# Optimization experiments

Hardware: AMD Instinct MI355X
Metric: run time of the kernel (lower is better)

## Reference

```python
import jax, jax.numpy as jnp
import numpy as np

N = 100000      # nodes
E = 600000      # edges
IN, OUT = 128, 32
L1 = IN - (IN - OUT) // 3          # 96
L2 = IN - (2 * (IN - OUT)) // 3    # 64


def setup_inputs() -> dict:
    key = jax.random.key(0)
    ks = jax.random.split(key, 12)

    def lin(k, i, o):
        return jax.random.normal(k, (i, o), jnp.float32) / np.float32(np.sqrt(i))

    return {
        "x": jax.random.normal(ks[0], (N, IN), jnp.float32),
        "edge_index": jax.random.randint(ks[1], (2, E), 0, N, dtype=jnp.int32),
        # ClusterGCNConv 1: lin_out (W,b) + lin_root (no bias)
        "W1": lin(ks[2], IN, L1), "b1": jnp.zeros((L1,), jnp.float32), "Wr1": lin(ks[3], IN, L1),
        # ClusterGCNConv 2
        "W2": lin(ks[4], L1, L2), "b2": jnp.zeros((L2,), jnp.float32), "Wr2": lin(ks[5], L1, L2),
        # GCNConv mu / logstd heads
        "Wmu": lin(ks[6], L2, OUT), "bmu": jnp.zeros((OUT,), jnp.float32),
        "Wls": lin(ks[7], L2, OUT), "bls": jnp.zeros((OUT,), jnp.float32),
    }


def _with_self_loops(edge_index, n):
    loops = jnp.arange(n, dtype=edge_index.dtype)
    src = jnp.concatenate([edge_index[0], loops])
    dst = jnp.concatenate([edge_index[1], loops])
    return src, dst


def _cluster_gcn(x, edge_index, W, b, Wr, n):
    # PyG ClusterGCNConv (diag_lambda=0): out = (D^{-1} (A+I)) x @ W + b + x @ Wr
    src, dst = _with_self_loops(edge_index, n)
    deg = jax.ops.segment_sum(jnp.ones_like(dst, x.dtype), dst, num_segments=n)
    dinv = 1.0 / jnp.clip(deg, 1.0)
    agg = jax.ops.segment_sum(x[src] * dinv[dst][:, None], dst, num_segments=n)
    return agg @ W + b + x @ Wr


def _gcn(x, edge_index, W, b, n):
    # PyG GCNConv: h = x @ W; out = D^{-1/2} (A+I) D^{-1/2} h + b
    h = x @ W
    src, dst = _with_self_loops(edge_index, n)
    deg = jax.ops.segment_sum(jnp.ones_like(dst, h.dtype), dst, num_segments=n)
    dis = jax.lax.rsqrt(jnp.clip(deg, 1.0))  # deg >= 1 thanks to self loops
    norm = dis[src] * dis[dst]
    return jax.ops.segment_sum(h[src] * norm[:, None], dst, num_segments=n) + b


def reference(x, edge_index, W1, b1, Wr1, W2, b2, Wr2, Wmu, bmu, Wls, bls):
    n = x.shape[0]
    h = jax.nn.relu(_cluster_gcn(x, edge_index, W1, b1, Wr1, n))
    h = jax.nn.relu(_cluster_gcn(h, edge_index, W2, b2, Wr2, n))
    return (_gcn(h, edge_index, Wmu, bmu, n), _gcn(h, edge_index, Wls, bls, n))
```

## Files before the change

### kernel.cpp

```cpp
#include <hip/hip_runtime.h>

#define TPB 256

typedef __attribute__((ext_vector_type(8))) short          bf8_t;
typedef __attribute__((ext_vector_type(8))) unsigned short us8_t;
typedef __attribute__((ext_vector_type(4))) float          f4_t;
typedef __attribute__((ext_vector_type(4))) unsigned short us4_t;

__device__ __forceinline__ unsigned short f2bf(float f) {
    union { float f; unsigned u; } v; v.f = f;
    unsigned r = v.u + 0x7FFFu + ((v.u >> 16) & 1u);
    return (unsigned short)(r >> 16);
}
__device__ __forceinline__ float bf2f(unsigned short u) {
    union { unsigned u; float f; } v; v.u = (unsigned)u << 16; return v.f;
}


__global__ void k_count(const int* __restrict__ ei, int E, int* __restrict__ cnt) {
    int e = blockIdx.x * TPB + threadIdx.x;
    if (e < E) atomicAdd(&cnt[ei[E + e]], 1);
}

__global__ void k_blocksum(const int* __restrict__ cnt, int n, int* __restrict__ bsum) {
    __shared__ int s[TPB];
    int t = threadIdx.x, i = blockIdx.x * TPB + t;
    s[t] = (i < n) ? cnt[i] : 0;
    __syncthreads();
    for (int off = TPB / 2; off > 0; off >>= 1) {
        if (t < off) s[t] += s[t + off];
        __syncthreads();
    }
    if (t == 0) bsum[blockIdx.x] = s[0];
}

__global__ void k_scan_bsum(int* __restrict__ bsum, int nb) {
    __shared__ int s[512];
    int t = threadIdx.x;
    int v = (t < nb) ? bsum[t] : 0;
    s[t] = v; __syncthreads();
    for (int off = 1; off < 512; off <<= 1) {
        int x = (t >= off) ? s[t - off] : 0;
        __syncthreads();
        s[t] += x;
        __syncthreads();
    }
    if (t < nb) bsum[t] = s[t] - v;
}

__global__ void k_rowptr(const int* __restrict__ cnt, const int* __restrict__ bsum, int n, int E,
                         int* __restrict__ rowptr, int* __restrict__ cursor,
                         float* __restrict__ dinv, float* __restrict__ dis) {
    __shared__ int s[TPB];
    int t = threadIdx.x, i = blockIdx.x * TPB + t;
    int v = (i < n) ? cnt[i] : 0;
    s[t] = v; __syncthreads();
    for (int off = 1; off < TPB; off <<= 1) {
        int x = (t >= off) ? s[t - off] : 0;
        __syncthreads();
        s[t] += x;
        __syncthreads();
    }
    if (i < n) {
        int start = bsum[blockIdx.x] + s[t] - v;
        rowptr[i] = start;
        cursor[i] = start;
        float d = (float)(v + 1);
        dinv[i] = 1.0f / d;
        dis[i]  = rsqrtf(d);
    }
    if (i == 0) rowptr[n] = E;
}

__global__ void k_fill(const int* __restrict__ ei, int E,
                       int* __restrict__ cursor, int* __restrict__ col) {
    int e = blockIdx.x * TPB + threadIdx.x;
    if (e < E) {
        int src = ei[e], dst = ei[E + e];
        int p = atomicAdd(&cursor[dst], 1);
        col[p] = src;
    }
}

__global__ void k_wconv(const float* W1, const float* Wr1, const float* W2, const float* Wr2,
                        const float* Wmu, const float* Wls,
                        unsigned short* T1, unsigned short* Tr1, unsigned short* T2,
                        unsigned short* Tr2, unsigned short* Tmu, unsigned short* Tls) {
    const float* W; unsigned short* T; int K, M;
    switch (blockIdx.y) {
        case 0: W = W1;  T = T1;  K = 128; M = 96; break;
        case 1: W = Wr1; T = Tr1; K = 128; M = 96; break;
        case 2: W = W2;  T = T2;  K = 96;  M = 64; break;
        case 3: W = Wr2; T = Tr2; K = 96;  M = 64; break;
        case 4: W = Wmu; T = Tmu; K = 64;  M = 32; break;
        default:W = Wls; T = Tls; K = 64;  M = 32; break;
    }
    int idx = blockIdx.x * TPB + threadIdx.x;
    if (idx < K * M) {
        int m = idx / K, k = idx % K;
        T[idx] = f2bf(W[k * M + m]);
    }
}

template <int K, int M, bool AF32>
__global__ __launch_bounds__(TPB) void k_gemm3(const void* __restrict__ Av,
                                               const unsigned short* __restrict__ WT,
                                               unsigned short* __restrict__ Yb,
                                               int n, int nt) {
    constexpr int KS = K / 32;
    constexpr int ST = K + 8;
    __shared__ unsigned short Bs[M * ST];
    for (int i = threadIdx.x * 8; i < M * K; i += TPB * 8) {
        int m = i / K, k = i - m * K;
        *(us8_t*)(Bs + m * ST + k) = *(const us8_t*)(WT + i);
    }
    __syncthreads();

    int lane = threadIdx.x & 63;
    int wave = threadIdx.x >> 6;
    int quad = lane >> 4;
    int l15  = lane & 15;

    for (int tile = blockIdx.x; tile < nt; tile += gridDim.x) {
        int base = tile * 64 + wave * 16;
        int rA = base + l15; if (rA > n - 1) rA = n - 1;

        bf8_t a[KS];
        if (AF32) {
            const float* ap = (const float*)Av + (size_t)rA * K + quad * 8;
#pragma unroll
            for (int s = 0; s < KS; s++) {
                f4_t lo = *(const f4_t*)(ap + s * 32);
                f4_t hi = *(const f4_t*)(ap + s * 32 + 4);
                bf8_t t;
                t[0] = (short)f2bf(lo.x); t[1] = (short)f2bf(lo.y);
                t[2] = (short)f2bf(lo.z); t[3] = (short)f2bf(lo.w);
                t[4] = (short)f2bf(hi.x); t[5] = (short)f2bf(hi.y);
                t[6] = (short)f2bf(hi.z); t[7] = (short)f2bf(hi.w);
                a[s] = t;
            }
        } else {
            const unsigned short* ap = (const unsigned short*)Av + (size_t)rA * K + quad * 8;
#pragma unroll
            for (int s = 0; s < KS; s++) a[s] = *(const bf8_t*)(ap + s * 32);
        }

        int row = base + quad * 4;
#pragma unroll
        for (int ct = 0; ct < M / 16; ct++) {
            const unsigned short* bp = Bs + (ct * 16 + l15) * ST + quad * 8;
            f4_t acc = {0.f, 0.f, 0.f, 0.f};
#pragma unroll
            for (int s = 0; s < KS; s++) {
                bf8_t b = *(const bf8_t*)(bp + s * 32);
                acc = __builtin_amdgcn_mfma_f32_16x16x32_bf16(a[s], b, acc, 0, 0, 0);
            }
            int colg = ct * 16 + l15;
#pragma unroll
            for (int r = 0; r < 4; r++) {
                if (row + r < n) Yb[(size_t)(row + r) * M + colg] = f2bf(acc[r]);
            }
        }
    }
}

__global__ __launch_bounds__(TPB, 4) void k_fuse1(const unsigned short* __restrict__ AB,
                                                  const unsigned short* __restrict__ WT2,
                                                  const float* __restrict__ bias,
                                                  const float* __restrict__ dinv,
                                                  const int* __restrict__ rowptr,
                                                  const int* __restrict__ col,
                                                  unsigned short* __restrict__ AB2,
                                                  int n, int nt) {
    constexpr int LDA = 192, MF = 96, ST1 = 104, KS = 3, M2 = 128;
    __shared__ unsigned short Hs[2][16 * ST1];

    int t = threadIdx.x;
    int lane = t & 63, wave = t >> 6, quad = lane >> 4, l15 = lane & 15;

    bf8_t breg[2][KS];
#pragma unroll
    for (int j = 0; j < 2; j++) {
        const unsigned short* bp = WT2 + (size_t)((wave * 2 + j) * 16 + l15) * 96 + quad * 8;
#pragma unroll
        for (int s = 0; s < KS; s++) breg[j][s] = *(const bf8_t*)(bp + s * 32);
    }

    int gl = t >> 4;
    int cg = t & 15;
    int c  = cg * 8;
    bool p1act = (c < MF);

    int p = 0;
    for (int tile = blockIdx.x; tile < nt; tile += gridDim.x, p ^= 1) {
        int tbase = tile * 16;
        if (p1act) {
            int g = tbase + gl; if (g > n - 1) g = n - 1;
            int r0 = rowptr[g], r1 = rowptr[g + 1];
            float acc[8];
            {
                bf8_t v = *(const bf8_t*)(AB + (size_t)g * LDA + c);
#pragma unroll
                for (int j = 0; j < 8; j++) acc[j] = bf2f((unsigned short)v[j]);
            }
            int e = r0;
            for (; e + 4 <= r1; e += 4) {
                int s0 = col[e], s1 = col[e + 1], s2 = col[e + 2], s3 = col[e + 3];
                bf8_t v0 = *(const bf8_t*)(AB + (size_t)s0 * LDA + c);
                bf8_t v1 = *(const bf8_t*)(AB + (size_t)s1 * LDA + c);
                bf8_t v2 = *(const bf8_t*)(AB + (size_t)s2 * LDA + c);
                bf8_t v3 = *(const bf8_t*)(AB + (size_t)s3 * LDA + c);
#pragma unroll
                for (int j = 0; j < 8; j++)
                    acc[j] += (bf2f((unsigned short)v0[j]) + bf2f((unsigned short)v1[j]))
                            + (bf2f((unsigned short)v2[j]) + bf2f((unsigned short)v3[j]));
            }
            for (; e < r1; ++e) {
                int s = col[e];
                bf8_t v = *(const bf8_t*)(AB + (size_t)s * LDA + c);
#pragma unroll
                for (int j = 0; j < 8; j++) acc[j] += bf2f((unsigned short)v[j]);
            }
            float di = dinv[g];
            bf8_t rr = *(const bf8_t*)(AB + (size_t)g * LDA + MF + c);
            us8_t o;
#pragma unroll
            for (int j = 0; j < 8; j++)
                o[j] = f2bf(fmaxf(acc[j] * di + bf2f((unsigned short)rr[j]) + bias[c + j], 0.f));
            *(us8_t*)(&Hs[p][gl * ST1 + c]) = o;
        }
        __syncthreads();

        int row = tbase + quad * 4;
#pragma unroll
        for (int j = 0; j < 2; j++) {
            const unsigned short* apl = &Hs[p][l15 * ST1 + quad * 8];
            f4_t acc2 = {0.f, 0.f, 0.f, 0.f};
#pragma unroll
            for (int s = 0; s < KS; s++) {
                bf8_t a = *(const bf8_t*)(apl + s * 32);
                acc2 = __builtin_amdgcn_mfma_f32_16x16x32_bf16(a, breg[j][s], acc2, 0, 0, 0);
            }
            int colg = (wave * 2 + j) * 16 + l15;
#pragma unroll
            for (int r = 0; r < 4; r++) {
                if (row + r < n) AB2[(size_t)(row + r) * M2 + colg] = f2bf(acc2[r]);
            }
        }
    }
}

template <int MF, int GRP, bool SCALE>
__global__ __launch_bounds__(TPB) void k_aggc(const unsigned short* __restrict__ AB,
                                              const float* __restrict__ bias,
                                              const float* __restrict__ dinv,
                                              const float* __restrict__ dis,
                                              const int* __restrict__ rowptr,
                                              const int* __restrict__ col,
                                              unsigned short* __restrict__ Hb, int n) {
    constexpr int LD = 2 * MF;
    int g = blockIdx.x * (TPB / GRP) + threadIdx.x / GRP;
    int l = threadIdx.x & (GRP - 1);
    if (g >= n) return;
    int c = l * 8;
    if (c >= MF) return;
    int r0 = rowptr[g], r1 = rowptr[g + 1];
    float acc[8];
    {
        bf8_t v = *(const bf8_t*)(AB + (size_t)g * LD + c);
#pragma unroll
        for (int j = 0; j < 8; j++) acc[j] = bf2f((unsigned short)v[j]);
    }
    int e = r0;
    for (; e + 4 <= r1; e += 4) {
        int s0 = col[e], s1 = col[e + 1], s2 = col[e + 2], s3 = col[e + 3];
        bf8_t v0 = *(const bf8_t*)(AB + (size_t)s0 * LD + c);
        bf8_t v1 = *(const bf8_t*)(AB + (size_t)s1 * LD + c);
        bf8_t v2 = *(const bf8_t*)(AB + (size_t)s2 * LD + c);
        bf8_t v3 = *(const bf8_t*)(AB + (size_t)s3 * LD + c);
#pragma unroll
        for (int j = 0; j < 8; j++)
            acc[j] += (bf2f((unsigned short)v0[j]) + bf2f((unsigned short)v1[j]))
                    + (bf2f((unsigned short)v2[j]) + bf2f((unsigned short)v3[j]));
    }
    for (; e < r1; ++e) {
        int s = col[e];
        bf8_t v = *(const bf8_t*)(AB + (size_t)s * LD + c);
#pragma unroll
        for (int j = 0; j < 8; j++) acc[j] += bf2f((unsigned short)v[j]);
    }
    float di = dinv[g];
    float sc = SCALE ? dis[g] : 1.0f;
    bf8_t rr = *(const bf8_t*)(AB + (size_t)g * LD + MF + c);
    us8_t o;
#pragma unroll
    for (int j = 0; j < 8; j++) {
        float h = fmaxf(acc[j] * di + bf2f((unsigned short)rr[j]) + bias[c + j], 0.f);
        o[j] = f2bf(SCALE ? sc * h : h);
    }
    *(us8_t*)(Hb + (size_t)g * MF + c) = o;
}

__global__ __launch_bounds__(TPB, 4) void k_fuse2(const unsigned short* __restrict__ H2s,
                                                  const unsigned short* __restrict__ WTo,
                                                  const float* __restrict__ bmu,
                                                  const float* __restrict__ bls,
                                                  const float* __restrict__ dis,
                                                  const int* __restrict__ rowptr,
                                                  const int* __restrict__ col,
                                                  float* __restrict__ out, int n, int nt) {
    constexpr int ST2 = 72, KS = 2;
    __shared__ unsigned short Zs[2][32 * ST2];

    int t = threadIdx.x;
    int lane = t & 63, wave = t >> 6, quad = lane >> 4, l15 = lane & 15;

    bf8_t breg[KS];
    {
        const unsigned short* bp = WTo + (size_t)(wave * 16 + l15) * 64 + quad * 8;
#pragma unroll
        for (int s = 0; s < KS; s++) breg[s] = *(const bf8_t*)(bp + s * 32);
    }
    int colg = wave * 16 + l15;
    float bias = (colg < 32) ? bmu[colg] : bls[colg - 32];
    float* dstc = (colg < 32) ? (out + colg) : (out + (size_t)n * 32 + (colg - 32));

    int gl = t >> 3;
    int c  = (t & 7) * 8;

    int p = 0;
    for (int tile = blockIdx.x; tile < nt; tile += gridDim.x, p ^= 1) {
        int tbase = tile * 32;
        {
            int g = tbase + gl; if (g > n - 1) g = n - 1;
            int r0 = rowptr[g], r1 = rowptr[g + 1];
            float acc[8];
            {
                bf8_t v = *(const bf8_t*)(H2s + (size_t)g * 64 + c);
#pragma unroll
                for (int j = 0; j < 8; j++) acc[j] = bf2f((unsigned short)v[j]);
            }
            int e = r0;
            for (; e + 4 <= r1; e += 4) {
                int s0 = col[e], s1 = col[e + 1], s2 = col[e + 2], s3 = col[e + 3];
                bf8_t v0 = *(const bf8_t*)(H2s + (size_t)s0 * 64 + c);
                bf8_t v1 = *(const bf8_t*)(H2s + (size_t)s1 * 64 + c);
                bf8_t v2 = *(const bf8_t*)(H2s + (size_t)s2 * 64 + c);
                bf8_t v3 = *(const bf8_t*)(H2s + (size_t)s3 * 64 + c);
#pragma unroll
                for (int j = 0; j < 8; j++)
                    acc[j] += (bf2f((unsigned short)v0[j]) + bf2f((unsigned short)v1[j]))
                            + (bf2f((unsigned short)v2[j]) + bf2f((unsigned short)v3[j]));
            }
            for (; e < r1; ++e) {
                int s = col[e];
                bf8_t v = *(const bf8_t*)(H2s + (size_t)s * 64 + c);
#pragma unroll
                for (int j = 0; j < 8; j++) acc[j] += bf2f((unsigned short)v[j]);
            }
            float dg = dis[g];
            us8_t o;
#pragma unroll
            for (int j = 0; j < 8; j++) o[j] = f2bf(dg * acc[j]);
            *(us8_t*)(&Zs[p][gl * ST2 + c]) = o;
        }
        __syncthreads();

#pragma unroll
        for (int st = 0; st < 2; st++) {
            const unsigned short* apl = &Zs[p][(st * 16 + l15) * ST2 + quad * 8];
            bf8_t a[KS];
#pragma unroll
            for (int s = 0; s < KS; s++) a[s] = *(const bf8_t*)(apl + s * 32);
            f4_t acc = {0.f, 0.f, 0.f, 0.f};
#pragma unroll
            for (int s = 0; s < KS; s++)
                acc = __builtin_amdgcn_mfma_f32_16x16x32_bf16(a[s], breg[s], acc, 0, 0, 0);
            int row = tbase + st * 16 + quad * 4;
#pragma unroll
            for (int r = 0; r < 4; r++) {
                if (row + r < n) dstc[(size_t)(row + r) * 32] = acc[r] + bias;
            }
        }
    }
}


extern "C" void kernel_launch(void* const* d_in, const int* in_sizes, int n_in,
                              void* d_out, int out_size, void* d_ws, size_t ws_size,
                              hipStream_t stream) {
    const float* x   = (const float*)d_in[0];
    const int*   ei  = (const int*)d_in[1];
    const float* W1  = (const float*)d_in[2];
    const float* b1  = (const float*)d_in[3];
    const float* Wr1 = (const float*)d_in[4];
    const float* W2  = (const float*)d_in[5];
    const float* b2  = (const float*)d_in[6];
    const float* Wr2 = (const float*)d_in[7];
    const float* Wmu = (const float*)d_in[8];
    const float* bmu = (const float*)d_in[9];
    const float* Wls = (const float*)d_in[10];
    const float* bls = (const float*)d_in[11];
    float* out = (float*)d_out;

    const int IN = 128, L1F = 96, L2F = 64;
    const int N = in_sizes[0] / IN;
    const int E = in_sizes[1] / 2;

    char* ws = (char*)d_ws;
    size_t off = 0;
    auto alloc = [&](size_t b) { size_t r = off; off += (b + 255) & ~(size_t)255; return r; };

    const int nb = (N + TPB - 1) / TPB;
    int*   cnt  = (int*)(ws + alloc((size_t)N * 4));
    int*   bsum = (int*)(ws + alloc((size_t)nb * 4));
    int*   rowp = (int*)(ws + alloc((size_t)(N + 1) * 4));
    int*   curs = (int*)(ws + alloc((size_t)N * 4));
    int*   col  = (int*)(ws + alloc((size_t)E * 4));
    float* dinv = (float*)(ws + alloc((size_t)N * 4));
    float* dis  = (float*)(ws + alloc((size_t)N * 4));
    unsigned short* T1  = (unsigned short*)(ws + alloc((size_t)IN  * L1F * 2));
    unsigned short* Tr1 = (unsigned short*)(ws + alloc((size_t)IN  * L1F * 2));
    unsigned short* T2  = (unsigned short*)(ws + alloc((size_t)L1F * L2F * 2));
    unsigned short* Tr2 = (unsigned short*)(ws + alloc((size_t)L1F * L2F * 2));
    unsigned short* Tmu = (unsigned short*)(ws + alloc((size_t)L2F * 32 * 2));
    unsigned short* Tls = (unsigned short*)(ws + alloc((size_t)L2F * 32 * 2));
    unsigned short* AB1 = (unsigned short*)(ws + alloc((size_t)N * 2 * L1F * 2));
    unsigned short* AB2 = (unsigned short*)(ws + alloc((size_t)N * 2 * L2F * 2));
    unsigned short* H2s = (unsigned short*)(ws + alloc((size_t)N * L2F * 2));
    (void)Tr1; (void)Tr2; (void)Tls;

    hipMemsetAsync(cnt, 0, (size_t)N * 4, stream);

    dim3 eg((E + TPB - 1) / TPB);
    k_count<<<eg, TPB, 0, stream>>>(ei, E, cnt);
    k_blocksum<<<nb, TPB, 0, stream>>>(cnt, N, bsum);
    k_scan_bsum<<<1, 512, 0, stream>>>(bsum, nb);
    k_rowptr<<<nb, TPB, 0, stream>>>(cnt, bsum, N, E, rowp, curs, dinv, dis);
    k_fill<<<eg, TPB, 0, stream>>>(ei, E, curs, col);

    k_wconv<<<dim3(48, 6), TPB, 0, stream>>>(W1, Wr1, W2, Wr2, Wmu, Wls,
                                             T1, Tr1, T2, Tr2, Tmu, Tls);

    const int nt64 = (N + 63) / 64;
    k_gemm3<128, 192, true><<<768, TPB, 0, stream>>>(x, T1, AB1, N, nt64);

    const int nt16 = (N + 15) / 16;
    k_fuse1<<<2048, TPB, 0, stream>>>(AB1, T2, b1, dinv, rowp, col, AB2, N, nt16);

    k_aggc<64, 8, true><<<(N + 31) / 32, TPB, 0, stream>>>(AB2, b2, dinv, dis, rowp, col, H2s, N);

    const int nt32 = (N + 31) / 32;
    k_fuse2<<<2048, TPB, 0, stream>>>(H2s, Tmu, bmu, bls, dis, rowp, col, out, N, nt32);
}
```

Baseline: 281.4 us.

## Split edge gathers across two lane groups per node and merge scan kernels

The three gather-aggregation kernels now split each node's edge list between two half-groups of lanes (even/odd edges) and combine the partial sums with a cross-lane shuffle. This doubles the memory-level parallelism per node and fills the lanes that were idle in k_fuse1, at the cost of extra shuffles and some wasted lanes on low-degree nodes. Separately, the block-sum and block-scan kernels are merged into one single-block kernel that sums each chunk serially, which removes a launch but adds serial work in one block.

Result: slower. 320.3 us (+13.9%).

```diff
diff --git a/kernel.cpp b/kernel.cpp
--- a/kernel.cpp
+++ b/kernel.cpp
@@ -22,30 +22,23 @@
     if (e < E) atomicAdd(&cnt[ei[E + e]], 1);
 }
 
-__global__ void k_blocksum(const int* __restrict__ cnt, int n, int* __restrict__ bsum) {
-    __shared__ int s[TPB];
-    int t = threadIdx.x, i = blockIdx.x * TPB + t;
-    s[t] = (i < n) ? cnt[i] : 0;
-    __syncthreads();
-    for (int off = TPB / 2; off > 0; off >>= 1) {
-        if (t < off) s[t] += s[t + off];
-        __syncthreads();
-    }
-    if (t == 0) bsum[blockIdx.x] = s[0];
-}
-
-__global__ void k_scan_bsum(int* __restrict__ bsum, int nb) {
+__global__ void k_scan12(const int* __restrict__ cnt, int n, int nb, int* __restrict__ bsum) {
     __shared__ int s[512];
     int t = threadIdx.x;
-    int v = (t < nb) ? bsum[t] : 0;
-    s[t] = v; __syncthreads();
+    int sum = 0;
+    if (t < nb) {
+        int base = t * TPB;
+        int end = base + TPB; if (end > n) end = n;
+        for (int i = base; i < end; i++) sum += cnt[i];
+    }
+    s[t] = sum; __syncthreads();
     for (int off = 1; off < 512; off <<= 1) {
         int x = (t >= off) ? s[t - off] : 0;
         __syncthreads();
         s[t] += x;
         __syncthreads();
     }
-    if (t < nb) bsum[t] = s[t] - v;
+    if (t < nb) bsum[t] = s[t] - sum;
 }
 
 __global__ void k_rowptr(const int* __restrict__ cnt, const int* __restrict__ bsum, int n, int E,
@@ -164,6 +157,7 @@
     }
 }
 
+
 __global__ __launch_bounds__(TPB, 4) void k_fuse1(const unsigned short* __restrict__ AB,
                                                   const unsigned short* __restrict__ WT2,
                                                   const float* __restrict__ bias,
@@ -186,48 +180,60 @@
         for (int s = 0; s < KS; s++) breg[j][s] = *(const bf8_t*)(bp + s * 32);
     }
 
-    int gl = t >> 4;
-    int cg = t & 15;
-    int c  = cg * 8;
-    bool p1act = (c < MF);
+    int u   = t & 31;
+    int eh  = u >> 4;
+    int cg  = u & 15;
+    int c   = cg * 8;
+    bool act = (c < MF);
+    int slot = t >> 5;
 
     int p = 0;
     for (int tile = blockIdx.x; tile < nt; tile += gridDim.x, p ^= 1) {
         int tbase = tile * 16;
-        if (p1act) {
+#pragma unroll
+        for (int pp = 0; pp < 2; pp++) {
+            int gl = pp * 8 + slot;
             int g = tbase + gl; if (g > n - 1) g = n - 1;
-            int r0 = rowptr[g], r1 = rowptr[g + 1];
             float acc[8];
-            {
-                bf8_t v = *(const bf8_t*)(AB + (size_t)g * LDA + c);
-#pragma unroll
-                for (int j = 0; j < 8; j++) acc[j] = bf2f((unsigned short)v[j]);
-            }
-            int e = r0;
-            for (; e + 4 <= r1; e += 4) {
-                int s0 = col[e], s1 = col[e + 1], s2 = col[e + 2], s3 = col[e + 3];
-                bf8_t v0 = *(const bf8_t*)(AB + (size_t)s0 * LDA + c);
-                bf8_t v1 = *(const bf8_t*)(AB + (size_t)s1 * LDA + c);
-                bf8_t v2 = *(const bf8_t*)(AB + (size_t)s2 * LDA + c);
-                bf8_t v3 = *(const bf8_t*)(AB + (size_t)s3 * LDA + c);
+#pragma unroll
+            for (int j = 0; j < 8; j++) acc[j] = 0.f;
+            if (act) {
+                if (eh == 0) {
+                    bf8_t v = *(const bf8_t*)(AB + (size_t)g * LDA + c);
+#pragma unroll
+                    for (int j = 0; j < 8; j++) acc[j] = bf2f((unsigned short)v[j]);
+                }
+                int r0 = rowptr[g], r1 = rowptr[g + 1];
+                int e = r0 + eh;
+                for (; e + 6 < r1; e += 8) {
+                    int s0 = col[e], s1 = col[e + 2], s2 = col[e + 4], s3 = col[e + 6];
+                    bf8_t v0 = *(const bf8_t*)(AB + (size_t)s0 * LDA + c);
+                    bf8_t v1 = *(const bf8_t*)(AB + (size_t)s1 * LDA + c);
+                    bf8_t v2 = *(const bf8_t*)(AB + (size_t)s2 * LDA + c);
+                    bf8_t v3 = *(const bf8_t*)(AB + (size_t)s3 * LDA + c);
+#pragma unroll
+                    for (int j = 0; j < 8; j++)
+                        acc[j] += (bf2f((unsigned short)v0[j]) + bf2f((unsigned short)v1[j]))
+                                + (bf2f((unsigned short)v2[j]) + bf2f((unsigned short)v3[j]));
+                }
+                for (; e < r1; e += 2) {
+                    int s = col[e];
+                    bf8_t v = *(const bf8_t*)(AB + (size_t)s * LDA + c);
+#pragma unroll
+                    for (int j = 0; j < 8; j++) acc[j] += bf2f((unsigned short)v[j]);
+                }
+            }
+#pragma unroll
+            for (int j = 0; j < 8; j++) acc[j] += __shfl_xor(acc[j], 16, 64);
+            if (act && eh == 0) {
+                float di = dinv[g];
+                bf8_t rr = *(const bf8_t*)(AB + (size_t)g * LDA + MF + c);
+                us8_t o;
 #pragma unroll
                 for (int j = 0; j < 8; j++)
-                    acc[j] += (bf2f((unsigned short)v0[j]) + bf2f((unsigned short)v1[j]))
-                            + (bf2f((unsigned short)v2[j]) + bf2f((unsigned short)v3[j]));
-            }
-            for (; e < r1; ++e) {
-                int s = col[e];
-                bf8_t v = *(const bf8_t*)(AB + (size_t)s * LDA + c);
-#pragma unroll
-                for (int j = 0; j < 8; j++) acc[j] += bf2f((unsigned short)v[j]);
-            }
-            float di = dinv[g];
-            bf8_t rr = *(const bf8_t*)(AB + (size_t)g * LDA + MF + c);
-            us8_t o;
-#pragma unroll
-            for (int j = 0; j < 8; j++)
-                o[j] = f2bf(fmaxf(acc[j] * di + bf2f((unsigned short)rr[j]) + bias[c + j], 0.f));
-            *(us8_t*)(&Hs[p][gl * ST1 + c]) = o;
+                    o[j] = f2bf(fmaxf(acc[j] * di + bf2f((unsigned short)rr[j]) + bias[c + j], 0.f));
+                *(us8_t*)(&Hs[p][gl * ST1 + c]) = o;
+            }
         }
         __syncthreads();
 
@@ -250,30 +256,32 @@
     }
 }
 
-template <int MF, int GRP, bool SCALE>
-__global__ __launch_bounds__(TPB) void k_aggc(const unsigned short* __restrict__ AB,
-                                              const float* __restrict__ bias,
-                                              const float* __restrict__ dinv,
-                                              const float* __restrict__ dis,
-                                              const int* __restrict__ rowptr,
-                                              const int* __restrict__ col,
-                                              unsigned short* __restrict__ Hb, int n) {
-    constexpr int LD = 2 * MF;
-    int g = blockIdx.x * (TPB / GRP) + threadIdx.x / GRP;
-    int l = threadIdx.x & (GRP - 1);
+__global__ __launch_bounds__(TPB) void k_aggc2(const unsigned short* __restrict__ AB,
+                                               const float* __restrict__ bias,
+                                               const float* __restrict__ dinv,
+                                               const float* __restrict__ dis,
+                                               const int* __restrict__ rowptr,
+                                               const int* __restrict__ col,
+                                               unsigned short* __restrict__ Hb, int n) {
+    constexpr int MF = 64, LD = 128;
+    int t = threadIdx.x;
+    int g = blockIdx.x * 16 + (t >> 4);
     if (g >= n) return;
-    int c = l * 8;
-    if (c >= MF) return;
+    int u  = t & 15;
+    int eh = u >> 3;
+    int c  = (u & 7) * 8;
     int r0 = rowptr[g], r1 = rowptr[g + 1];
     float acc[8];
-    {
+#pragma unroll
+    for (int j = 0; j < 8; j++) acc[j] = 0.f;
+    if (eh == 0) {
         bf8_t v = *(const bf8_t*)(AB + (size_t)g * LD + c);
 #pragma unroll
         for (int j = 0; j < 8; j++) acc[j] = bf2f((unsigned short)v[j]);
     }
-    int e = r0;
-    for (; e + 4 <= r1; e += 4) {
-        int s0 = col[e], s1 = col[e + 1], s2 = col[e + 2], s3 = col[e + 3];
+    int e = r0 + eh;
+    for (; e + 6 < r1; e += 8) {
+        int s0 = col[e], s1 = col[e + 2], s2 = col[e + 4], s3 = col[e + 6];
         bf8_t v0 = *(const bf8_t*)(AB + (size_t)s0 * LD + c);
         bf8_t v1 = *(const bf8_t*)(AB + (size_t)s1 * LD + c);
         bf8_t v2 = *(const bf8_t*)(AB + (size_t)s2 * LD + c);
@@ -283,22 +291,25 @@
             acc[j] += (bf2f((unsigned short)v0[j]) + bf2f((unsigned short)v1[j]))
                     + (bf2f((unsigned short)v2[j]) + bf2f((unsigned short)v3[j]));
     }
-    for (; e < r1; ++e) {
+    for (; e < r1; e += 2) {
         int s = col[e];
         bf8_t v = *(const bf8_t*)(AB + (size_t)s * LD + c);
 #pragma unroll
         for (int j = 0; j < 8; j++) acc[j] += bf2f((unsigned short)v[j]);
     }
-    float di = dinv[g];
-    float sc = SCALE ? dis[g] : 1.0f;
-    bf8_t rr = *(const bf8_t*)(AB + (size_t)g * LD + MF + c);
-    us8_t o;
-#pragma unroll
-    for (int j = 0; j < 8; j++) {
-        float h = fmaxf(acc[j] * di + bf2f((unsigned short)rr[j]) + bias[c + j], 0.f);
-        o[j] = f2bf(SCALE ? sc * h : h);
-    }
-    *(us8_t*)(Hb + (size_t)g * MF + c) = o;
+#pragma unroll
+    for (int j = 0; j < 8; j++) acc[j] += __shfl_xor(acc[j], 8, 64);
+    if (eh == 0) {
+        float di = dinv[g], sc = dis[g];
+        bf8_t rr = *(const bf8_t*)(AB + (size_t)g * LD + MF + c);
+        us8_t o;
+#pragma unroll
+        for (int j = 0; j < 8; j++) {
+            float h = fmaxf(acc[j] * di + bf2f((unsigned short)rr[j]) + bias[c + j], 0.f);
+            o[j] = f2bf(sc * h);
+        }
+        *(us8_t*)(Hb + (size_t)g * MF + c) = o;
+    }
 }
 
 __global__ __launch_bounds__(TPB, 4) void k_fuse2(const unsigned short* __restrict__ H2s,
@@ -325,24 +336,30 @@
     float bias = (colg < 32) ? bmu[colg] : bls[colg - 32];
     float* dstc = (colg < 32) ? (out + colg) : (out + (size_t)n * 32 + (colg - 32));
 
-    int gl = t >> 3;
-    int c  = (t & 7) * 8;
+    int u  = t & 15;
+    int eh = u >> 3;
+    int c  = (u & 7) * 8;
+    int slot = t >> 4;
 
     int p = 0;
     for (int tile = blockIdx.x; tile < nt; tile += gridDim.x, p ^= 1) {
         int tbase = tile * 32;
-        {
+#pragma unroll
+        for (int pp = 0; pp < 2; pp++) {
+            int gl = pp * 16 + slot;
             int g = tbase + gl; if (g > n - 1) g = n - 1;
+            float acc[8];
+#pragma unroll
+            for (int j = 0; j < 8; j++) acc[j] = 0.f;
+            if (eh == 0) {
+                bf8_t v = *(const bf8_t*)(H2s + (size_t)g * 64 + c);
+#pragma unroll
+                for (int j = 0; j < 8; j++) acc[j] = bf2f((unsigned short)v[j]);
+            }
             int r0 = rowptr[g], r1 = rowptr[g + 1];
-            float acc[8];
-            {
-                bf8_t v = *(const bf8_t*)(H2s + (size_t)g * 64 + c);
-#pragma unroll
-                for (int j = 0; j < 8; j++) acc[j] = bf2f((unsigned short)v[j]);
-            }
-            int e = r0;
-            for (; e + 4 <= r1; e += 4) {
-                int s0 = col[e], s1 = col[e + 1], s2 = col[e + 2], s3 = col[e + 3];
+            int e = r0 + eh;
+            for (; e + 6 < r1; e += 8) {
+                int s0 = col[e], s1 = col[e + 2], s2 = col[e + 4], s3 = col[e + 6];
                 bf8_t v0 = *(const bf8_t*)(H2s + (size_t)s0 * 64 + c);
                 bf8_t v1 = *(const bf8_t*)(H2s + (size_t)s1 * 64 + c);
                 bf8_t v2 = *(const bf8_t*)(H2s + (size_t)s2 * 64 + c);
@@ -352,17 +369,21 @@
                     acc[j] += (bf2f((unsigned short)v0[j]) + bf2f((unsigned short)v1[j]))
                             + (bf2f((unsigned short)v2[j]) + bf2f((unsigned short)v3[j]));
             }
-            for (; e < r1; ++e) {
+            for (; e < r1; e += 2) {
                 int s = col[e];
                 bf8_t v = *(const bf8_t*)(H2s + (size_t)s * 64 + c);
 #pragma unroll
                 for (int j = 0; j < 8; j++) acc[j] += bf2f((unsigned short)v[j]);
             }
-            float dg = dis[g];
-            us8_t o;
-#pragma unroll
-            for (int j = 0; j < 8; j++) o[j] = f2bf(dg * acc[j]);
-            *(us8_t*)(&Zs[p][gl * ST2 + c]) = o;
+#pragma unroll
+            for (int j = 0; j < 8; j++) acc[j] += __shfl_xor(acc[j], 8, 64);
+            if (eh == 0) {
+                float dg = dis[g];
+                us8_t o;
+#pragma unroll
+                for (int j = 0; j < 8; j++) o[j] = f2bf(dg * acc[j]);
+                *(us8_t*)(&Zs[p][gl * ST2 + c]) = o;
+            }
         }
         __syncthreads();
 
@@ -434,8 +455,7 @@
 
     dim3 eg((E + TPB - 1) / TPB);
     k_count<<<eg, TPB, 0, stream>>>(ei, E, cnt);
-    k_blocksum<<<nb, TPB, 0, stream>>>(cnt, N, bsum);
-    k_scan_bsum<<<1, 512, 0, stream>>>(bsum, nb);
+    k_scan12<<<1, 512, 0, stream>>>(cnt, N, nb, bsum);
     k_rowptr<<<nb, TPB, 0, stream>>>(cnt, bsum, N, E, rowp, curs, dinv, dis);
     k_fill<<<eg, TPB, 0, stream>>>(ei, E, curs, col);
 
@@ -448,7 +468,7 @@
     const int nt16 = (N + 15) / 16;
     k_fuse1<<<2048, TPB, 0, stream>>>(AB1, T2, b1, dinv, rowp, col, AB2, N, nt16);
 
-    k_aggc<64, 8, true><<<(N + 31) / 32, TPB, 0, stream>>>(AB2, b2, dinv, dis, rowp, col, H2s, N);
+    k_aggc2<<<(N + 15) / 16, TPB, 0, stream>>>(AB2, b2, dinv, dis, rowp, col, H2s, N);
 
     const int nt32 = (N + 31) / 32;
     k_fuse2<<<2048, TPB, 0, stream>>>(H2s, Tmu, bmu, bls, dis, rowp, col, out, N, nt32);
```

## Split interleaved agg/root GEMM outputs into separate buffers and merge scan kernels

Applied to the files above, without the earlier changes.

The GEMM outputs that feed neighbour aggregation (Y) are now stored apart from the root-term outputs (R), each in its own dense buffer, instead of interleaved rows of width 2*F. Gathers over neighbours then read compact rows, so each gathered row spans fewer cache lines and the unused root half is no longer pulled in. The block-sum and block-scan kernels are also merged into one single-block kernel, removing a launch at the cost of a serial per-thread summation.

Measured after the change: 289.8 us. +3.0%, slower.

```diff
diff --git a/kernel.cpp b/kernel.cpp
--- a/kernel.cpp
+++ b/kernel.cpp
@@ -6,6 +6,7 @@
 typedef __attribute__((ext_vector_type(8))) unsigned short us8_t;
 typedef __attribute__((ext_vector_type(4))) float          f4_t;
 typedef __attribute__((ext_vector_type(4))) unsigned short us4_t;
+typedef __attribute__((ext_vector_type(4))) int            i4_t;
 
 __device__ __forceinline__ unsigned short f2bf(float f) {
     union { float f; unsigned u; } v; v.f = f;
@@ -22,30 +23,28 @@
     if (e < E) atomicAdd(&cnt[ei[E + e]], 1);
 }
 
-__global__ void k_blocksum(const int* __restrict__ cnt, int n, int* __restrict__ bsum) {
-    __shared__ int s[TPB];
-    int t = threadIdx.x, i = blockIdx.x * TPB + t;
-    s[t] = (i < n) ? cnt[i] : 0;
-    __syncthreads();
-    for (int off = TPB / 2; off > 0; off >>= 1) {
-        if (t < off) s[t] += s[t + off];
-        __syncthreads();
-    }
-    if (t == 0) bsum[blockIdx.x] = s[0];
-}
-
-__global__ void k_scan_bsum(int* __restrict__ bsum, int nb) {
+__global__ void k_scan12(const int* __restrict__ cnt, int n, int nb, int* __restrict__ bsum) {
     __shared__ int s[512];
     int t = threadIdx.x;
-    int v = (t < nb) ? bsum[t] : 0;
-    s[t] = v; __syncthreads();
+    int sum = 0;
+    if (t < nb) {
+        int base = t * TPB;
+        int end = base + TPB; if (end > n) end = n;
+        int i = base;
+        for (; i + 4 <= end; i += 4) {
+            i4_t v = *(const i4_t*)(cnt + i);
+            sum += v.x + v.y + v.z + v.w;
+        }
+        for (; i < end; i++) sum += cnt[i];
+    }
+    s[t] = sum; __syncthreads();
     for (int off = 1; off < 512; off <<= 1) {
         int x = (t >= off) ? s[t - off] : 0;
         __syncthreads();
         s[t] += x;
         __syncthreads();
     }
-    if (t < nb) bsum[t] = s[t] - v;
+    if (t < nb) bsum[t] = s[t] - sum;
 }
 
 __global__ void k_rowptr(const int* __restrict__ cnt, const int* __restrict__ bsum, int n, int E,
@@ -102,11 +101,12 @@
     }
 }
 
-template <int K, int M, bool AF32>
-__global__ __launch_bounds__(TPB) void k_gemm3(const void* __restrict__ Av,
-                                               const unsigned short* __restrict__ WT,
-                                               unsigned short* __restrict__ Yb,
-                                               int n, int nt) {
+template <int K, int M, int MH, bool AF32>
+__global__ __launch_bounds__(TPB) void k_gemm3s(const void* __restrict__ Av,
+                                                const unsigned short* __restrict__ WT,
+                                                unsigned short* __restrict__ Yb,
+                                                unsigned short* __restrict__ Rb,
+                                                int n, int nt) {
     constexpr int KS = K / 32;
     constexpr int ST = K + 8;
     __shared__ unsigned short Bs[M * ST];
@@ -156,23 +156,30 @@
                 acc = __builtin_amdgcn_mfma_f32_16x16x32_bf16(a[s], b, acc, 0, 0, 0);
             }
             int colg = ct * 16 + l15;
+            unsigned short* dst;
+            if (ct * 16 < MH) dst = Yb + (size_t)0 * MH + colg;
+            else              dst = Rb + (colg - MH);
+            constexpr int SY = MH, SR = M - MH;
+            int stride = (ct * 16 < MH) ? SY : SR;
 #pragma unroll
             for (int r = 0; r < 4; r++) {
-                if (row + r < n) Yb[(size_t)(row + r) * M + colg] = f2bf(acc[r]);
-            }
-        }
-    }
-}
-
-__global__ __launch_bounds__(TPB, 4) void k_fuse1(const unsigned short* __restrict__ AB,
+                if (row + r < n) dst[(size_t)(row + r) * stride] = f2bf(acc[r]);
+            }
+        }
+    }
+}
+
+__global__ __launch_bounds__(TPB, 4) void k_fuse1(const unsigned short* __restrict__ Y1,
+                                                  const unsigned short* __restrict__ R1,
                                                   const unsigned short* __restrict__ WT2,
                                                   const float* __restrict__ bias,
                                                   const float* __restrict__ dinv,
                                                   const int* __restrict__ rowptr,
                                                   const int* __restrict__ col,
-                                                  unsigned short* __restrict__ AB2,
+                                                  unsigned short* __restrict__ Y2,
+                                                  unsigned short* __restrict__ R2,
                                                   int n, int nt) {
-    constexpr int LDA = 192, MF = 96, ST1 = 104, KS = 3, M2 = 128;
+    constexpr int MF = 96, ST1 = 104, KS = 3;
     __shared__ unsigned short Hs[2][16 * ST1];
 
     int t = threadIdx.x;
@@ -199,17 +206,17 @@
             int r0 = rowptr[g], r1 = rowptr[g + 1];
             float acc[8];
             {
-                bf8_t v = *(const bf8_t*)(AB + (size_t)g * LDA + c);
+                bf8_t v = *(const bf8_t*)(Y1 + (size_t)g * MF + c);
 #pragma unroll
                 for (int j = 0; j < 8; j++) acc[j] = bf2f((unsigned short)v[j]);
             }
             int e = r0;
             for (; e + 4 <= r1; e += 4) {
                 int s0 = col[e], s1 = col[e + 1], s2 = col[e + 2], s3 = col[e + 3];
-                bf8_t v0 = *(const bf8_t*)(AB + (size_t)s0 * LDA + c);
-                bf8_t v1 = *(const bf8_t*)(AB + (size_t)s1 * LDA + c);
-                bf8_t v2 = *(const bf8_t*)(AB + (size_t)s2 * LDA + c);
-                bf8_t v3 = *(const bf8_t*)(AB + (size_t)s3 * LDA + c);
+                bf8_t v0 = *(const bf8_t*)(Y1 + (size_t)s0 * MF + c);
+                bf8_t v1 = *(const bf8_t*)(Y1 + (size_t)s1 * MF + c);
+                bf8_t v2 = *(const bf8_t*)(Y1 + (size_t)s2 * MF + c);
+                bf8_t v3 = *(const bf8_t*)(Y1 + (size_t)s3 * MF + c);
 #pragma unroll
                 for (int j = 0; j < 8; j++)
                     acc[j] += (bf2f((unsigned short)v0[j]) + bf2f((unsigned short)v1[j]))
@@ -217,12 +224,12 @@
             }
             for (; e < r1; ++e) {
                 int s = col[e];
-                bf8_t v = *(const bf8_t*)(AB + (size_t)s * LDA + c);
+                bf8_t v = *(const bf8_t*)(Y1 + (size_t)s * MF + c);
 #pragma unroll
                 for (int j = 0; j < 8; j++) acc[j] += bf2f((unsigned short)v[j]);
             }
             float di = dinv[g];
-            bf8_t rr = *(const bf8_t*)(AB + (size_t)g * LDA + MF + c);
+            bf8_t rr = *(const bf8_t*)(R1 + (size_t)g * MF + c);
             us8_t o;
 #pragma unroll
             for (int j = 0; j < 8; j++)
@@ -242,42 +249,41 @@
                 acc2 = __builtin_amdgcn_mfma_f32_16x16x32_bf16(a, breg[j][s], acc2, 0, 0, 0);
             }
             int colg = (wave * 2 + j) * 16 + l15;
+            unsigned short* dst = (colg < 64) ? (Y2 + colg) : (R2 + (colg - 64));
 #pragma unroll
             for (int r = 0; r < 4; r++) {
-                if (row + r < n) AB2[(size_t)(row + r) * M2 + colg] = f2bf(acc2[r]);
-            }
-        }
-    }
-}
-
-template <int MF, int GRP, bool SCALE>
-__global__ __launch_bounds__(TPB) void k_aggc(const unsigned short* __restrict__ AB,
-                                              const float* __restrict__ bias,
-                                              const float* __restrict__ dinv,
-                                              const float* __restrict__ dis,
-                                              const int* __restrict__ rowptr,
-                                              const int* __restrict__ col,
-                                              unsigned short* __restrict__ Hb, int n) {
-    constexpr int LD = 2 * MF;
+                if (row + r < n) dst[(size_t)(row + r) * 64] = f2bf(acc2[r]);
+            }
+        }
+    }
+}
+
+__global__ __launch_bounds__(TPB) void k_aggc2(const unsigned short* __restrict__ Y2,
+                                               const unsigned short* __restrict__ R2,
+                                               const float* __restrict__ bias,
+                                               const float* __restrict__ dinv,
+                                               const float* __restrict__ dis,
+                                               const int* __restrict__ rowptr,
+                                               const int* __restrict__ col,
+                                               unsigned short* __restrict__ Hb, int n) {
+    constexpr int MF = 64, GRP = 8;
     int g = blockIdx.x * (TPB / GRP) + threadIdx.x / GRP;
-    int l = threadIdx.x & (GRP - 1);
     if (g >= n) return;
-    int c = l * 8;
-    if (c >= MF) return;
+    int c = (threadIdx.x & (GRP - 1)) * 8;
     int r0 = rowptr[g], r1 = rowptr[g + 1];
     float acc[8];
     {
-        bf8_t v = *(const bf8_t*)(AB + (size_t)g * LD + c);
+        bf8_t v = *(const bf8_t*)(Y2 + (size_t)g * MF + c);
 #pragma unroll
         for (int j = 0; j < 8; j++) acc[j] = bf2f((unsigned short)v[j]);
     }
     int e = r0;
     for (; e + 4 <= r1; e += 4) {
         int s0 = col[e], s1 = col[e + 1], s2 = col[e + 2], s3 = col[e + 3];
-        bf8_t v0 = *(const bf8_t*)(AB + (size_t)s0 * LD + c);
-        bf8_t v1 = *(const bf8_t*)(AB + (size_t)s1 * LD + c);
-        bf8_t v2 = *(const bf8_t*)(AB + (size_t)s2 * LD + c);
-        bf8_t v3 = *(const bf8_t*)(AB + (size_t)s3 * LD + c);
+        bf8_t v0 = *(const bf8_t*)(Y2 + (size_t)s0 * MF + c);
+        bf8_t v1 = *(const bf8_t*)(Y2 + (size_t)s1 * MF + c);
+        bf8_t v2 = *(const bf8_t*)(Y2 + (size_t)s2 * MF + c);
+        bf8_t v3 = *(const bf8_t*)(Y2 + (size_t)s3 * MF + c);
 #pragma unroll
         for (int j = 0; j < 8; j++)
             acc[j] += (bf2f((unsigned short)v0[j]) + bf2f((unsigned short)v1[j]))
@@ -285,18 +291,17 @@
     }
     for (; e < r1; ++e) {
         int s = col[e];
-        bf8_t v = *(const bf8_t*)(AB + (size_t)s * LD + c);
+        bf8_t v = *(const bf8_t*)(Y2 + (size_t)s * MF + c);
 #pragma unroll
         for (int j = 0; j < 8; j++) acc[j] += bf2f((unsigned short)v[j]);
     }
-    float di = dinv[g];
-    float sc = SCALE ? dis[g] : 1.0f;
-    bf8_t rr = *(const bf8_t*)(AB + (size_t)g * LD + MF + c);
+    float di = dinv[g], sc = dis[g];
+    bf8_t rr = *(const bf8_t*)(R2 + (size_t)g * MF + c);
     us8_t o;
 #pragma unroll
     for (int j = 0; j < 8; j++) {
         float h = fmaxf(acc[j] * di + bf2f((unsigned short)rr[j]) + bias[c + j], 0.f);
-        o[j] = f2bf(SCALE ? sc * h : h);
+        o[j] = f2bf(sc * h);
     }
     *(us8_t*)(Hb + (size_t)g * MF + c) = o;
 }
@@ -425,8 +430,10 @@
     unsigned short* Tr2 = (unsigned short*)(ws + alloc((size_t)L1F * L2F * 2));
     unsigned short* Tmu = (unsigned short*)(ws + alloc((size_t)L2F * 32 * 2));
     unsigned short* Tls = (unsigned short*)(ws + alloc((size_t)L2F * 32 * 2));
-    unsigned short* AB1 = (unsigned short*)(ws + alloc((size_t)N * 2 * L1F * 2));
-    unsigned short* AB2 = (unsigned short*)(ws + alloc((size_t)N * 2 * L2F * 2));
+    unsigned short* Y1  = (unsigned short*)(ws + alloc((size_t)N * L1F * 2));
+    unsigned short* R1  = (unsigned short*)(ws + alloc((size_t)N * L1F * 2));
+    unsigned short* Y2  = (unsigned short*)(ws + alloc((size_t)N * L2F * 2));
+    unsigned short* R2  = (unsigned short*)(ws + alloc((size_t)N * L2F * 2));
     unsigned short* H2s = (unsigned short*)(ws + alloc((size_t)N * L2F * 2));
     (void)Tr1; (void)Tr2; (void)Tls;
 
@@ -434,8 +441,7 @@
 
     dim3 eg((E + TPB - 1) / TPB);
     k_count<<<eg, TPB, 0, stream>>>(ei, E, cnt);
-    k_blocksum<<<nb, TPB, 0, stream>>>(cnt, N, bsum);
-    k_scan_bsum<<<1, 512, 0, stream>>>(bsum, nb);
+    k_scan12<<<1, 512, 0, stream>>>(cnt, N, nb, bsum);
     k_rowptr<<<nb, TPB, 0, stream>>>(cnt, bsum, N, E, rowp, curs, dinv, dis);
     k_fill<<<eg, TPB, 0, stream>>>(ei, E, curs, col);
 
@@ -443,12 +449,12 @@
                                              T1, Tr1, T2, Tr2, Tmu, Tls);
 
     const int nt64 = (N + 63) / 64;
-    k_gemm3<128, 192, true><<<768, TPB, 0, stream>>>(x, T1, AB1, N, nt64);
+    k_gemm3s<128, 192, 96, true><<<768, TPB, 0, stream>>>(x, T1, Y1, R1, N, nt64);
 
     const int nt16 = (N + 15) / 16;
-    k_fuse1<<<2048, TPB, 0, stream>>>(AB1, T2, b1, dinv, rowp, col, AB2, N, nt16);
-
-    k_aggc<64, 8, true><<<(N + 31) / 32, TPB, 0, stream>>>(AB2, b2, dinv, dis, rowp, col, H2s, N);
+    k_fuse1<<<2048, TPB, 0, stream>>>(Y1, R1, T2, b1, dinv, rowp, col, Y2, R2, N, nt16);
+
+    k_aggc2<<<(N + 31) / 32, TPB, 0, stream>>>(Y2, R2, b2, dinv, dis, rowp, col, H2s, N);
 
     const int nt32 = (N + 31) / 32;
     k_fuse2<<<2048, TPB, 0, stream>>>(H2s, Tmu, bmu, bls, dis, rowp, col, out, N, nt32);
```

## Merge degree block-sum and scan kernels; persistent 512-thread GEMM over 16-row tiles

Applied to the files above, without the earlier changes.

Replaces the separate block-sum and block-scan kernels with a single one-block kernel, where each thread sums one 256-entry chunk of the counts and the block then scans those sums. This removes one launch. The first-layer GEMM now runs as 256 persistent blocks of 512 threads (8 waves), and each wave independently strides over 16-row tiles. The aim is fewer weight-to-LDS loads per block and better load balance. The trade-off is launch_bounds(512,1), which limits occupancy to one block per CU, and a serial single-block reduction over 100k counts.

Measured after the change: 288.2 us. +2.4%, slower.

```diff
diff --git a/kernel.cpp b/kernel.cpp
--- a/kernel.cpp
+++ b/kernel.cpp
@@ -6,6 +6,7 @@
 typedef __attribute__((ext_vector_type(8))) unsigned short us8_t;
 typedef __attribute__((ext_vector_type(4))) float          f4_t;
 typedef __attribute__((ext_vector_type(4))) unsigned short us4_t;
+typedef __attribute__((ext_vector_type(4))) int            i4_t;
 
 __device__ __forceinline__ unsigned short f2bf(float f) {
     union { float f; unsigned u; } v; v.f = f;
@@ -22,30 +23,28 @@
     if (e < E) atomicAdd(&cnt[ei[E + e]], 1);
 }
 
-__global__ void k_blocksum(const int* __restrict__ cnt, int n, int* __restrict__ bsum) {
-    __shared__ int s[TPB];
-    int t = threadIdx.x, i = blockIdx.x * TPB + t;
-    s[t] = (i < n) ? cnt[i] : 0;
-    __syncthreads();
-    for (int off = TPB / 2; off > 0; off >>= 1) {
-        if (t < off) s[t] += s[t + off];
-        __syncthreads();
-    }
-    if (t == 0) bsum[blockIdx.x] = s[0];
-}
-
-__global__ void k_scan_bsum(int* __restrict__ bsum, int nb) {
+__global__ void k_scan12(const int* __restrict__ cnt, int n, int nb, int* __restrict__ bsum) {
     __shared__ int s[512];
     int t = threadIdx.x;
-    int v = (t < nb) ? bsum[t] : 0;
-    s[t] = v; __syncthreads();
+    int sum = 0;
+    if (t < nb) {
+        int base = t * TPB;
+        int end = base + TPB; if (end > n) end = n;
+        int i = base;
+        for (; i + 4 <= end; i += 4) {
+            i4_t v = *(const i4_t*)(cnt + i);
+            sum += v.x + v.y + v.z + v.w;
+        }
+        for (; i < end; i++) sum += cnt[i];
+    }
+    s[t] = sum; __syncthreads();
     for (int off = 1; off < 512; off <<= 1) {
         int x = (t >= off) ? s[t - off] : 0;
         __syncthreads();
         s[t] += x;
         __syncthreads();
     }
-    if (t < nb) bsum[t] = s[t] - v;
+    if (t < nb) bsum[t] = s[t] - sum;
 }
 
 __global__ void k_rowptr(const int* __restrict__ cnt, const int* __restrict__ bsum, int n, int E,
@@ -103,14 +102,14 @@
 }
 
 template <int K, int M, bool AF32>
-__global__ __launch_bounds__(TPB) void k_gemm3(const void* __restrict__ Av,
-                                               const unsigned short* __restrict__ WT,
-                                               unsigned short* __restrict__ Yb,
-                                               int n, int nt) {
+__global__ __launch_bounds__(512, 1) void k_gemm9(const void* __restrict__ Av,
+                                                  const unsigned short* __restrict__ WT,
+                                                  unsigned short* __restrict__ Yb,
+                                                  int n, int nt) {
     constexpr int KS = K / 32;
     constexpr int ST = K + 8;
     __shared__ unsigned short Bs[M * ST];
-    for (int i = threadIdx.x * 8; i < M * K; i += TPB * 8) {
+    for (int i = threadIdx.x * 8; i < M * K; i += 512 * 8) {
         int m = i / K, k = i - m * K;
         *(us8_t*)(Bs + m * ST + k) = *(const us8_t*)(WT + i);
     }
@@ -121,9 +120,9 @@
     int quad = lane >> 4;
     int l15  = lane & 15;
 
-    for (int tile = blockIdx.x; tile < nt; tile += gridDim.x) {
-        int base = tile * 64 + wave * 16;
-        int rA = base + l15; if (rA > n - 1) rA = n - 1;
+    for (int t = blockIdx.x * 8 + wave; t < nt; t += gridDim.x * 8) {
+        int tbase = t * 16;
+        int rA = tbase + l15; if (rA > n - 1) rA = n - 1;
 
         bf8_t a[KS];
         if (AF32) {
@@ -132,12 +131,12 @@
             for (int s = 0; s < KS; s++) {
                 f4_t lo = *(const f4_t*)(ap + s * 32);
                 f4_t hi = *(const f4_t*)(ap + s * 32 + 4);
-                bf8_t t;
-                t[0] = (short)f2bf(lo.x); t[1] = (short)f2bf(lo.y);
-                t[2] = (short)f2bf(lo.z); t[3] = (short)f2bf(lo.w);
-                t[4] = (short)f2bf(hi.x); t[5] = (short)f2bf(hi.y);
-                t[6] = (short)f2bf(hi.z); t[7] = (short)f2bf(hi.w);
-                a[s] = t;
+                bf8_t tv;
+                tv[0] = (short)f2bf(lo.x); tv[1] = (short)f2bf(lo.y);
+                tv[2] = (short)f2bf(lo.z); tv[3] = (short)f2bf(lo.w);
+                tv[4] = (short)f2bf(hi.x); tv[5] = (short)f2bf(hi.y);
+                tv[6] = (short)f2bf(hi.z); tv[7] = (short)f2bf(hi.w);
+                a[s] = tv;
             }
         } else {
             const unsigned short* ap = (const unsigned short*)Av + (size_t)rA * K + quad * 8;
@@ -145,7 +144,7 @@
             for (int s = 0; s < KS; s++) a[s] = *(const bf8_t*)(ap + s * 32);
         }
 
-        int row = base + quad * 4;
+        int row = tbase + quad * 4;
 #pragma unroll
         for (int ct = 0; ct < M / 16; ct++) {
             const unsigned short* bp = Bs + (ct * 16 + l15) * ST + quad * 8;
@@ -434,18 +433,16 @@
 
     dim3 eg((E + TPB - 1) / TPB);
     k_count<<<eg, TPB, 0, stream>>>(ei, E, cnt);
-    k_blocksum<<<nb, TPB, 0, stream>>>(cnt, N, bsum);
-    k_scan_bsum<<<1, 512, 0, stream>>>(bsum, nb);
+    k_scan12<<<1, 512, 0, stream>>>(cnt, N, nb, bsum);
     k_rowptr<<<nb, TPB, 0, stream>>>(cnt, bsum, N, E, rowp, curs, dinv, dis);
     k_fill<<<eg, TPB, 0, stream>>>(ei, E, curs, col);
 
     k_wconv<<<dim3(48, 6), TPB, 0, stream>>>(W1, Wr1, W2, Wr2, Wmu, Wls,
                                              T1, Tr1, T2, Tr2, Tmu, Tls);
 
-    const int nt64 = (N + 63) / 64;
-    k_gemm3<128, 192, true><<<768, TPB, 0, stream>>>(x, T1, AB1, N, nt64);
-
     const int nt16 = (N + 15) / 16;
+    k_gemm9<128, 192, true><<<256, 512, 0, stream>>>(x, T1, AB1, N, nt16);
+
     k_fuse1<<<2048, TPB, 0, stream>>>(AB1, T2, b1, dinv, rowp, col, AB2, N, nt16);
 
     k_aggc<64, 8, true><<<(N + 31) / 32, TPB, 0, stream>>>(AB2, b2, dinv, dis, rowp, col, H2s, N);
```
